# Performance work log

Hardware: AMD Instinct MI355X
Metric: run time of the kernel (lower is better)

## Reference

```python
import jax, jax.numpy as jnp
import numpy as np

N = 50000      # nodes
E = 600000     # edges
C = 128        # in_channels
H = 128        # hidden_channels
O = 128        # out_channels
G = 512        # graphs in batch
BN_EPS = 1e-5


def setup_inputs() -> dict:
    key = jax.random.key(0)
    ks = jax.random.split(key, 16)

    def w(k, shape):
        return jax.random.normal(k, shape, dtype=jnp.float32) * 0.05

    inp = {}
    inp["x"] = jax.random.normal(ks[0], (N, C), dtype=jnp.float32)
    inp["edge_index"] = jax.random.randint(ks[1], (2, E), 0, N, dtype=jnp.int64)
    inp["batch"] = jnp.sort(jax.random.randint(ks[2], (N,), 0, G, dtype=jnp.int64))

    dims = [(C, H, H), (H, H, H), (H, H, O)]
    ki = 3
    for li, (din, dh, dout) in enumerate(dims, 1):
        inp[f"g{li}_W1"] = w(ks[ki], (din, dh)); inp[f"g{li}_b1"] = jnp.zeros((dh,), jnp.float32)
        inp[f"g{li}_gm"] = jnp.ones((dh,), jnp.float32); inp[f"g{li}_bt"] = jnp.zeros((dh,), jnp.float32)
        inp[f"g{li}_rm"] = jnp.zeros((dh,), jnp.float32); inp[f"g{li}_rv"] = jnp.ones((dh,), jnp.float32)
        inp[f"g{li}_W2"] = w(ks[ki + 1], (dh, dout)); inp[f"g{li}_b2"] = jnp.zeros((dout,), jnp.float32)
        ki += 2
    inp["lin_W"] = w(ks[ki], (H + H + O, O))
    inp["lin_b"] = jnp.zeros((O,), jnp.float32)
    return inp


def gin_conv(x, src, dst, W1, b1, gm, bt, rm, rv, W2, b2):
    # GINConv (eps=0): mlp(x + sum_{j in N(i)} x_j); mlp = Linear-BN(eval)-ReLU-Linear
    agg = jax.ops.segment_sum(x[src], dst, num_segments=N)   # [N, d] scatter-add
    h = (x + agg) @ W1 + b1
    h = (h - rm) * jax.lax.rsqrt(rv + BN_EPS) * gm + bt      # BatchNorm1d, eval mode
    return jax.nn.relu(h) @ W2 + b2


def reference(x, edge_index, batch,
              g1_W1, g1_b1, g1_gm, g1_bt, g1_rm, g1_rv, g1_W2, g1_b2,
              g2_W1, g2_b1, g2_gm, g2_bt, g2_rm, g2_rv, g2_W2, g2_b2,
              g3_W1, g3_b1, g3_gm, g3_bt, g3_rm, g3_rv, g3_W2, g3_b2,
              lin_W, lin_b):
    src, dst = edge_index[0], edge_index[1]
    # dropout(0.2) is identity in eval mode
    x1 = jax.nn.relu(gin_conv(x, src, dst, g1_W1, g1_b1, g1_gm, g1_bt, g1_rm, g1_rv, g1_W2, g1_b2))
    x2 = jax.nn.relu(gin_conv(x1, src, dst, g2_W1, g2_b1, g2_gm, g2_bt, g2_rm, g2_rv, g2_W2, g2_b2))
    x3 = gin_conv(x2, src, dst, g3_W1, g3_b1, g3_gm, g3_bt, g3_rm, g3_rv, g3_W2, g3_b2)
    xc = jnp.concatenate([x1, x2, x3], axis=-1)              # JumpingKnowledge 'cat' -> [N, H+H+O]
    sums = jax.ops.segment_sum(xc, batch, num_segments=G)    # global_mean_pool
    cnt = jax.ops.segment_sum(jnp.ones((N, 1), xc.dtype), batch, num_segments=G)
    pooled = sums / jnp.maximum(cnt, 1.0)                    # [G, H+H+O]
    return pooled @ lin_W + lin_b                            # [G, O]
```

## Files before the change

### kernel.cpp

```cpp
#include <hip/hip_runtime.h>
#include <hip/hip_bf16.h>

#define NNODES 50000
#define NEDGES 600000
#define NGRAPHS 512
#define BN_EPS 1e-5f

typedef short bf16x8 __attribute__((ext_vector_type(8)));
typedef float f32x4 __attribute__((ext_vector_type(4)));

__device__ __forceinline__ void bf_split(float x, ushort& h, ushort& l) {
    __hip_bfloat16 bh = __float2bfloat16(x);
    float r = x - __bfloat162float(bh);
    __hip_bfloat16 bl = __float2bfloat16(r);
    h = __builtin_bit_cast(ushort, bh);
    l = __builtin_bit_cast(ushort, bl);
}
__device__ __forceinline__ ushort f2b(float x) {
    return __builtin_bit_cast(ushort, __float2bfloat16(x));
}
__device__ __forceinline__ float b2f(ushort u) {
    union { uint i; float f; } c; c.i = ((uint)u) << 16; return c.f;
}

__global__ __launch_bounds__(256) void prep_kernel(
    const float* __restrict__ x, ushort* __restrict__ xh,
    float* __restrict__ pooled, const int* __restrict__ dst,
    int* __restrict__ counts, int* __restrict__ row_ptr,
    const float* W0, const float* W1, const float* W2, const float* W3,
    const float* W4, const float* W5, ushort* __restrict__ hi, ushort* __restrict__ lo) {
    int b = blockIdx.x, t = threadIdx.x;
    if (b < 3125) {
        int f4 = b * 512 + t * 2;
        float4 a0 = ((const float4*)x)[f4];
        float4 a1 = ((const float4*)x)[f4 + 1];
        ushort4 u0 = {f2b(a0.x), f2b(a0.y), f2b(a0.z), f2b(a0.w)};
        ushort4 u1 = {f2b(a1.x), f2b(a1.y), f2b(a1.z), f2b(a1.w)};
        int e0 = f4 * 4;
        *(ushort4*)(xh + e0) = u0;
        *(ushort4*)(xh + e0 + 4) = u1;
        if (b == 0 && t == 0) row_ptr[NNODES] = NEDGES;
    } else if (b < 3317) {
        ((float4*)pooled)[(b - 3125) * 256 + t] = make_float4(0.f, 0.f, 0.f, 0.f);
    } else if (b < 5661) {
        int i = (b - 3317) * 256 + t;
        if (i < NEDGES) atomicAdd(&counts[dst[i]], 1);
    } else {
        int wb = b - 5661;
        const float* Ws[6] = {W0, W1, W2, W3, W4, W5};
        const float* W = Ws[wb >> 4];
        ushort* h = hi + (size_t)(wb >> 4) * 16384;
        ushort* l = lo + (size_t)(wb >> 4) * 16384;
        int chunk = wb & 15;
#pragma unroll
        for (int i = 0; i < 4; i++) {
            int idx = chunk * 1024 + i * 256 + t;
            int j    = idx & 7;
            int lane = (idx >> 3) & 63;
            int nt   = (idx >> 9) & 7;
            int kb   = (idx >> 12) & 3;
            int k = kb * 32 + ((lane >> 4) << 3) + j;
            int n = nt * 16 + (lane & 15);
            ushort hh, ll;
            bf_split(W[k * 128 + n], hh, ll);
            h[idx] = hh;
            l[idx] = ll;
        }
    }
}

__global__ __launch_bounds__(256) void scan1_kernel(const int* __restrict__ counts,
                                                    int* __restrict__ partials, int n) {
    __shared__ int s[256];
    int i = blockIdx.x * 256 + threadIdx.x;
    int v = (i < n) ? counts[i] : 0;
    s[threadIdx.x] = v;
    __syncthreads();
    for (int off = 128; off > 0; off >>= 1) {
        if (threadIdx.x < off) s[threadIdx.x] += s[threadIdx.x + off];
        __syncthreads();
    }
    if (threadIdx.x == 0) partials[blockIdx.x] = s[0];
}

__global__ __launch_bounds__(256) void scan3_kernel(const int* __restrict__ counts,
                                                    const int* __restrict__ partials,
                                                    int* __restrict__ row_ptr,
                                                    int* __restrict__ cursor, int n, int nb) {
    __shared__ int s[256];
    __shared__ int base_sh;
    int t = threadIdx.x;
    int pv = (t < (int)blockIdx.x && t < nb) ? partials[t] : 0;
    s[t] = pv;
    __syncthreads();
    for (int off = 128; off > 0; off >>= 1) {
        if (t < off) s[t] += s[t + off];
        __syncthreads();
    }
    if (t == 0) base_sh = s[0];
    __syncthreads();
    int base = base_sh;
    int i = blockIdx.x * 256 + t;
    int v = (i < n) ? counts[i] : 0;
    __syncthreads();
    s[t] = v;
    __syncthreads();
    for (int off = 1; off < 256; off <<= 1) {
        int nv = (t >= off) ? s[t - off] : 0;
        __syncthreads();
        s[t] += nv;
        __syncthreads();
    }
    if (i < n) {
        int ex = base + s[t] - v;
        row_ptr[i] = ex;
        cursor[i] = ex;
    }
}

__global__ __launch_bounds__(256) void scatter_kernel(const int* __restrict__ src,
                                                      const int* __restrict__ dst,
                                                      int* __restrict__ cursor,
                                                      int* __restrict__ esrc, int E) {
    int i = blockIdx.x * 256 + threadIdx.x;
    if (i < E) {
        int p = atomicAdd(&cursor[dst[i]], 1);
        esrc[p] = src[i];
    }
}

#define GB8(ACC, E0)                                                            \
    {                                                                           \
        int i0 = esrc[E0],     i1 = esrc[E0 + 1], i2 = esrc[E0 + 2], i3 = esrc[E0 + 3]; \
        int i4 = esrc[E0 + 4], i5 = esrc[E0 + 5], i6 = esrc[E0 + 6], i7 = esrc[E0 + 7]; \
        ushort4 v0 = xv[(size_t)i0 * 32 + q];                                   \
        ushort4 v1 = xv[(size_t)i1 * 32 + q];                                   \
        ushort4 v2 = xv[(size_t)i2 * 32 + q];                                   \
        ushort4 v3 = xv[(size_t)i3 * 32 + q];                                   \
        ushort4 v4 = xv[(size_t)i4 * 32 + q];                                   \
        ushort4 v5 = xv[(size_t)i5 * 32 + q];                                   \
        ushort4 v6 = xv[(size_t)i6 * 32 + q];                                   \
        ushort4 v7 = xv[(size_t)i7 * 32 + q];                                   \
        ACC.x += ((b2f(v0.x) + b2f(v1.x)) + (b2f(v2.x) + b2f(v3.x))) +          \
                 ((b2f(v4.x) + b2f(v5.x)) + (b2f(v6.x) + b2f(v7.x)));           \
        ACC.y += ((b2f(v0.y) + b2f(v1.y)) + (b2f(v2.y) + b2f(v3.y))) +          \
                 ((b2f(v4.y) + b2f(v5.y)) + (b2f(v6.y) + b2f(v7.y)));           \
        ACC.z += ((b2f(v0.z) + b2f(v1.z)) + (b2f(v2.z) + b2f(v3.z))) +          \
                 ((b2f(v4.z) + b2f(v5.z)) + (b2f(v6.z) + b2f(v7.z)));           \
        ACC.w += ((b2f(v0.w) + b2f(v1.w)) + (b2f(v2.w) + b2f(v3.w))) +          \
                 ((b2f(v4.w) + b2f(v5.w)) + (b2f(v6.w) + b2f(v7.w)));           \
    }

template <bool RELU_OUT, bool WRITE_PLANES>
__global__ __launch_bounds__(128) void layer_kernel(
    const ushort* __restrict__ Pin,
    const int* __restrict__ rp, const int* __restrict__ esrc,
    const ushort* __restrict__ W1hi, const ushort* __restrict__ W1lo,
    const ushort* __restrict__ W2hi, const ushort* __restrict__ W2lo,
    const float* __restrict__ b1, const float* __restrict__ gm,
    const float* __restrict__ bt, const float* __restrict__ rm,
    const float* __restrict__ rv, const float* __restrict__ b2,
    ushort* __restrict__ Ch,
    const int* __restrict__ batch, float* __restrict__ pooled, int poff, int M) {
    __shared__ __align__(16) ushort smem[64 * 136];
    __shared__ int bsm[64];
    const int t = threadIdx.x;
    const int lane = t & 63;
    const int wv = t >> 6;
    const int row0 = blockIdx.x * 64;
    const int g = lane >> 4, c = lane & 15;

    if (t < 64) bsm[t] = (row0 + t < M) ? batch[row0 + t] : -1;

    {
        const int hw = t >> 5;
        const int q  = t & 31;
        const ushort4* xv = (const ushort4*)Pin;
        for (int i = 0; i < 16; i += 2) {
            const int mA = hw * 16 + i, mB = mA + 1;
            const int nA = row0 + mA, nB = row0 + mB;
            float4 aA = make_float4(0.f, 0.f, 0.f, 0.f);
            float4 aB = make_float4(0.f, 0.f, 0.f, 0.f);
            int eA = 0, endA = 0, eB = 0, endB = 0;
            if (nA < M) {
                ushort4 s = xv[(size_t)nA * 32 + q];
                aA.x = b2f(s.x); aA.y = b2f(s.y); aA.z = b2f(s.z); aA.w = b2f(s.w);
                eA = rp[nA]; endA = rp[nA + 1];
            }
            if (nB < M) {
                ushort4 s = xv[(size_t)nB * 32 + q];
                aB.x = b2f(s.x); aB.y = b2f(s.y); aB.z = b2f(s.z); aB.w = b2f(s.w);
                eB = rp[nB]; endB = rp[nB + 1];
            }
            while (eA + 8 <= endA && eB + 8 <= endB) {
                int a0 = esrc[eA],     a1 = esrc[eA + 1], a2 = esrc[eA + 2], a3 = esrc[eA + 3];
                int a4 = esrc[eA + 4], a5 = esrc[eA + 5], a6 = esrc[eA + 6], a7 = esrc[eA + 7];
                int b0 = esrc[eB],     b1_ = esrc[eB + 1], b2_ = esrc[eB + 2], b3 = esrc[eB + 3];
                int b4 = esrc[eB + 4], b5 = esrc[eB + 5], b6 = esrc[eB + 6], b7 = esrc[eB + 7];
                ushort4 uA0 = xv[(size_t)a0 * 32 + q], uA1 = xv[(size_t)a1 * 32 + q];
                ushort4 uA2 = xv[(size_t)a2 * 32 + q], uA3 = xv[(size_t)a3 * 32 + q];
                ushort4 uA4 = xv[(size_t)a4 * 32 + q], uA5 = xv[(size_t)a5 * 32 + q];
                ushort4 uA6 = xv[(size_t)a6 * 32 + q], uA7 = xv[(size_t)a7 * 32 + q];
                ushort4 uB0 = xv[(size_t)b0 * 32 + q], uB1 = xv[(size_t)b1_ * 32 + q];
                ushort4 uB2 = xv[(size_t)b2_ * 32 + q], uB3 = xv[(size_t)b3 * 32 + q];
                ushort4 uB4 = xv[(size_t)b4 * 32 + q], uB5 = xv[(size_t)b5 * 32 + q];
                ushort4 uB6 = xv[(size_t)b6 * 32 + q], uB7 = xv[(size_t)b7 * 32 + q];
                aA.x += ((b2f(uA0.x) + b2f(uA1.x)) + (b2f(uA2.x) + b2f(uA3.x))) +
                        ((b2f(uA4.x) + b2f(uA5.x)) + (b2f(uA6.x) + b2f(uA7.x)));
                aA.y += ((b2f(uA0.y) + b2f(uA1.y)) + (b2f(uA2.y) + b2f(uA3.y))) +
                        ((b2f(uA4.y) + b2f(uA5.y)) + (b2f(uA6.y) + b2f(uA7.y)));
                aA.z += ((b2f(uA0.z) + b2f(uA1.z)) + (b2f(uA2.z) + b2f(uA3.z))) +
                        ((b2f(uA4.z) + b2f(uA5.z)) + (b2f(uA6.z) + b2f(uA7.z)));
                aA.w += ((b2f(uA0.w) + b2f(uA1.w)) + (b2f(uA2.w) + b2f(uA3.w))) +
                        ((b2f(uA4.w) + b2f(uA5.w)) + (b2f(uA6.w) + b2f(uA7.w)));
                aB.x += ((b2f(uB0.x) + b2f(uB1.x)) + (b2f(uB2.x) + b2f(uB3.x))) +
                        ((b2f(uB4.x) + b2f(uB5.x)) + (b2f(uB6.x) + b2f(uB7.x)));
                aB.y += ((b2f(uB0.y) + b2f(uB1.y)) + (b2f(uB2.y) + b2f(uB3.y))) +
                        ((b2f(uB4.y) + b2f(uB5.y)) + (b2f(uB6.y) + b2f(uB7.y)));
                aB.z += ((b2f(uB0.z) + b2f(uB1.z)) + (b2f(uB2.z) + b2f(uB3.z))) +
                        ((b2f(uB4.z) + b2f(uB5.z)) + (b2f(uB6.z) + b2f(uB7.z)));
                aB.w += ((b2f(uB0.w) + b2f(uB1.w)) + (b2f(uB2.w) + b2f(uB3.w))) +
                        ((b2f(uB4.w) + b2f(uB5.w)) + (b2f(uB6.w) + b2f(uB7.w)));
                eA += 8; eB += 8;
            }
            for (; eA + 8 <= endA; eA += 8) GB8(aA, eA);
            for (; eB + 8 <= endB; eB += 8) GB8(aB, eB);
            for (; eA + 2 <= endA; eA += 2) {
                int i0 = esrc[eA], i1 = esrc[eA + 1];
                ushort4 v0 = xv[(size_t)i0 * 32 + q];
                ushort4 v1 = xv[(size_t)i1 * 32 + q];
                aA.x += b2f(v0.x) + b2f(v1.x); aA.y += b2f(v0.y) + b2f(v1.y);
                aA.z += b2f(v0.z) + b2f(v1.z); aA.w += b2f(v0.w) + b2f(v1.w);
            }
            for (; eA < endA; eA++) {
                ushort4 v = xv[(size_t)esrc[eA] * 32 + q];
                aA.x += b2f(v.x); aA.y += b2f(v.y); aA.z += b2f(v.z); aA.w += b2f(v.w);
            }
            for (; eB + 2 <= endB; eB += 2) {
                int i0 = esrc[eB], i1 = esrc[eB + 1];
                ushort4 v0 = xv[(size_t)i0 * 32 + q];
                ushort4 v1 = xv[(size_t)i1 * 32 + q];
                aB.x += b2f(v0.x) + b2f(v1.x); aB.y += b2f(v0.y) + b2f(v1.y);
                aB.z += b2f(v0.z) + b2f(v1.z); aB.w += b2f(v0.w) + b2f(v1.w);
            }
            for (; eB < endB; eB++) {
                ushort4 v = xv[(size_t)esrc[eB] * 32 + q];
                aB.x += b2f(v.x); aB.y += b2f(v.y); aB.z += b2f(v.z); aB.w += b2f(v.w);
            }
            ushort4 hA = {f2b(aA.x), f2b(aA.y), f2b(aA.z), f2b(aA.w)};
            ushort4 hB = {f2b(aB.x), f2b(aB.y), f2b(aB.z), f2b(aB.w)};
            *(ushort4*)&smem[(q >> 3) * 2048 + mA * 32 + (q & 7) * 4] = hA;
            *(ushort4*)&smem[(q >> 3) * 2048 + mB * 32 + (q & 7) * 4] = hB;
        }
    }
    __syncthreads();

    f32x4 acc[4][4];
#pragma unroll
    for (int i = 0; i < 4; i++)
#pragma unroll
        for (int j = 0; j < 4; j++) acc[i][j] = (f32x4){0.f, 0.f, 0.f, 0.f};

    for (int kb = 0; kb < 4; kb++) {
        bf16x8 bh[4], bl[4];
#pragma unroll
        for (int ct = 0; ct < 4; ct++) {
            const size_t wo = (((size_t)kb * 8 + (wv * 4 + ct)) * 64 + lane) * 8;
            bh[ct] = *(const bf16x8*)(W1hi + wo);
            bl[ct] = *(const bf16x8*)(W1lo + wo);
        }
        bf16x8 ah[4];
#pragma unroll
        for (int rt = 0; rt < 4; rt++) {
            int off = kb * 2048 + (rt * 16 + c) * 32 + g * 8;
            ah[rt] = *(bf16x8*)&smem[off];
        }
#pragma unroll
        for (int rt = 0; rt < 4; rt++)
#pragma unroll
            for (int ct = 0; ct < 4; ct++) {
                acc[rt][ct] = __builtin_amdgcn_mfma_f32_16x16x32_bf16(ah[rt], bh[ct], acc[rt][ct], 0, 0, 0);
                acc[rt][ct] = __builtin_amdgcn_mfma_f32_16x16x32_bf16(ah[rt], bl[ct], acc[rt][ct], 0, 0, 0);
            }
    }
    __syncthreads();

    {
        float cs[4], ca[4];
#pragma unroll
        for (int ct = 0; ct < 4; ct++) {
            int n = wv * 64 + ct * 16 + c;
            float s = gm[n] * rsqrtf(rv[n] + BN_EPS);
            cs[ct] = s;
            ca[ct] = (b1[n] - rm[n]) * s + bt[n];
        }
#pragma unroll
        for (int rt = 0; rt < 4; rt++)
#pragma unroll
            for (int r = 0; r < 4; r++) {
                int row = rt * 16 + g * 4 + r;
#pragma unroll
                for (int ct = 0; ct < 4; ct++) {
                    int col = wv * 64 + ct * 16 + c;
                    float v = fmaxf(acc[rt][ct][r] * cs[ct] + ca[ct], 0.f);
                    smem[row * 136 + col] = f2b(v);
                }
            }
    }
    __syncthreads();

#pragma unroll
    for (int i = 0; i < 4; i++)
#pragma unroll
        for (int j = 0; j < 4; j++) acc[i][j] = (f32x4){0.f, 0.f, 0.f, 0.f};

    for (int kb = 0; kb < 4; kb++) {
        bf16x8 bh[4], bl[4];
#pragma unroll
        for (int ct = 0; ct < 4; ct++) {
            const size_t wo = (((size_t)kb * 8 + (wv * 4 + ct)) * 64 + lane) * 8;
            bh[ct] = *(const bf16x8*)(W2hi + wo);
            bl[ct] = *(const bf16x8*)(W2lo + wo);
        }
        bf16x8 ah[4];
#pragma unroll
        for (int rt = 0; rt < 4; rt++) {
            int off = (rt * 16 + c) * 136 + kb * 32 + g * 8;
            ah[rt] = *(bf16x8*)&smem[off];
        }
#pragma unroll
        for (int rt = 0; rt < 4; rt++)
#pragma unroll
            for (int ct = 0; ct < 4; ct++) {
                acc[rt][ct] = __builtin_amdgcn_mfma_f32_16x16x32_bf16(ah[rt], bh[ct], acc[rt][ct], 0, 0, 0);
                acc[rt][ct] = __builtin_amdgcn_mfma_f32_16x16x32_bf16(ah[rt], bl[ct], acc[rt][ct], 0, 0, 0);
            }
    }
    __syncthreads();

    {
        float ca2[4];
#pragma unroll
        for (int ct = 0; ct < 4; ct++) ca2[ct] = b2[wv * 64 + ct * 16 + c];
#pragma unroll
        for (int rt = 0; rt < 4; rt++)
#pragma unroll
            for (int r = 0; r < 4; r++) {
                int rl = rt * 16 + g * 4 + r;
                int row = row0 + rl;
                bool valid = row < M;
#pragma unroll
                for (int ct = 0; ct < 4; ct++) {
                    int col = wv * 64 + ct * 16 + c;
                    float v = acc[rt][ct][r] + ca2[ct];
                    if (RELU_OUT) v = fmaxf(v, 0.f);
                    ushort hh = f2b(valid ? v : 0.f);
                    smem[rl * 136 + col] = hh;
                    if (WRITE_PLANES && valid) Ch[(size_t)row * 128 + col] = hh;
                }
            }
    }
    __syncthreads();

    {
        int col = t;
        int gcur = bsm[0];
        float accp = 0.f;
#pragma unroll 8
        for (int r = 0; r < 64; r++) {
            int gg = bsm[r];
            if (gg != gcur) {
                if (gcur >= 0) atomicAdd(&pooled[gcur * 384 + poff + col], accp);
                accp = 0.f;
                gcur = gg;
            }
            accp += b2f(smem[r * 136 + col]);
        }
        if (gcur >= 0) atomicAdd(&pooled[gcur * 384 + poff + col], accp);
    }
}

__global__ __launch_bounds__(128) void final_kernel(const float* __restrict__ pooled,
                                                    const int* __restrict__ batch,
                                                    const float* __restrict__ W,
                                                    const float* __restrict__ b,
                                                    float* __restrict__ out, int n) {
    __shared__ float ps[384];
    int gph = blockIdx.x, t = threadIdx.x;
    int lo1 = 0, hi1 = n;
    while (lo1 < hi1) { int mid = (lo1 + hi1) >> 1; if (batch[mid] < gph) lo1 = mid + 1; else hi1 = mid; }
    int start = lo1;
    int lo2 = start, hi2 = n;
    while (lo2 < hi2) { int mid = (lo2 + hi2) >> 1; if (batch[mid] < gph + 1) lo2 = mid + 1; else hi2 = mid; }
    int cnt = lo2 - start;
    float inv = 1.f / (float)(cnt > 0 ? cnt : 1);
    for (int i = t; i < 384; i += 128) ps[i] = pooled[gph * 384 + i] * inv;
    __syncthreads();
    float acc = b[t];
#pragma unroll 8
    for (int k = 0; k < 384; k++) acc += ps[k] * W[k * 128 + t];
    out[gph * 128 + t] = acc;
}

extern "C" void kernel_launch(void* const* d_in, const int* in_sizes, int n_in,
                              void* d_out, int out_size, void* d_ws, size_t ws_size,
                              hipStream_t stream) {
    const float* x     = (const float*)d_in[0];
    const int*   edge  = (const int*)d_in[1];
    const int*   batch = (const int*)d_in[2];
    const float* p[32];
    for (int i = 0; i < n_in && i < 32; i++) p[i] = (const float*)d_in[i];
    const float* lin_W = p[27];
    const float* lin_b = p[28];

    char* w = (char*)d_ws;
    auto alloc = [&](size_t bytes) { void* r = (void*)w; w += (bytes + 255) & ~(size_t)255; return r; };
    const size_t PL = (size_t)NNODES * 128;
    ushort* xh0   = (ushort*)alloc(PL * 2);
    ushort* p1h   = (ushort*)alloc(PL * 2);
    ushort* p2h   = xh0;
    float* pooled = (float*)alloc((size_t)NGRAPHS * 384 * 4);
    int* counts   = (int*)alloc((size_t)NNODES * 4);
    int* cursor   = (int*)alloc((size_t)NNODES * 4);
    int* row_ptr  = (int*)alloc((size_t)(NNODES + 1) * 4);
    int* esrc     = (int*)alloc((size_t)NEDGES * 4);
    int* partials = (int*)alloc(256 * 4);
    ushort* wt_hi = (ushort*)alloc((size_t)6 * 16384 * 2);
    ushort* wt_lo = (ushort*)alloc((size_t)6 * 16384 * 2);

    const int* src = edge;
    const int* dst = edge + NEDGES;

    hipMemsetAsync(counts, 0, (size_t)NNODES * 4, stream);
    prep_kernel<<<5757, 256, 0, stream>>>(x, xh0, pooled, dst, counts, row_ptr,
                                          p[3], p[9], p[11], p[17], p[19], p[25],
                                          wt_hi, wt_lo);

    int nb = (NNODES + 255) / 256;
    scan1_kernel<<<nb, 256, 0, stream>>>(counts, partials, NNODES);
    scan3_kernel<<<nb, 256, 0, stream>>>(counts, partials, row_ptr, cursor, NNODES, nb);
    scatter_kernel<<<(NEDGES + 255) / 256, 256, 0, stream>>>(src, dst, cursor, esrc, NEDGES);

    int grid = (NNODES + 63) / 64;
    layer_kernel<true, true><<<grid, 128, 0, stream>>>(xh0, row_ptr, esrc,
        wt_hi + 0 * 16384, wt_lo + 0 * 16384, wt_hi + 1 * 16384, wt_lo + 1 * 16384,
        p[4], p[5], p[6], p[7], p[8], p[10], p1h, batch, pooled, 0, NNODES);
    layer_kernel<true, true><<<grid, 128, 0, stream>>>(p1h, row_ptr, esrc,
        wt_hi + 2 * 16384, wt_lo + 2 * 16384, wt_hi + 3 * 16384, wt_lo + 3 * 16384,
        p[12], p[13], p[14], p[15], p[16], p[18], p2h, batch, pooled, 128, NNODES);
    layer_kernel<false, false><<<grid, 128, 0, stream>>>(p2h, row_ptr, esrc,
        wt_hi + 4 * 16384, wt_lo + 4 * 16384, wt_hi + 5 * 16384, wt_lo + 5 * 16384,
        p[20], p[21], p[22], p[23], p[24], p[26], nullptr, batch, pooled, 256, NNODES);

    final_kernel<<<NGRAPHS, 128, 0, stream>>>(pooled, batch, lin_W, lin_b,
                                              (float*)d_out, NNODES);
}
```

Baseline: 411.5 us.

## Widen gather loads to 16 bytes, use 4 waves per block, fuse scan

The neighbor gather now reads 8 bf16 values per lane with uint4 loads, so 16 lanes cover a row instead of 32. This makes fewer, wider memory transactions. Each layer block now runs 4 waves (256 threads) instead of 2, and each wave computes a 32-column MFMA slice instead of 64. That lowers per-thread accumulator registers and puts more waves in flight. The two-pass scan is merged into one kernel that recomputes the prefix of the counts on every block, removing a launch but doing redundant reads that grow with the block index.

```diff
diff --git a/kernel.cpp b/kernel.cpp
--- a/kernel.cpp
+++ b/kernel.cpp
@@ -22,6 +22,64 @@
 __device__ __forceinline__ float b2f(ushort u) {
     union { uint i; float f; } c; c.i = ((uint)u) << 16; return c.f;
 }
+__device__ __forceinline__ float blo(uint u) {
+    union { uint i; float f; } c; c.i = u << 16; return c.f;
+}
+__device__ __forceinline__ float bhi(uint u) {
+    union { uint i; float f; } c; c.i = u & 0xffff0000u; return c.f;
+}
+
+#define TREE8(A, v0, v1, v2, v3, v4, v5, v6, v7)                               \
+    A[0] += ((blo(v0.x) + blo(v1.x)) + (blo(v2.x) + blo(v3.x))) +              \
+            ((blo(v4.x) + blo(v5.x)) + (blo(v6.x) + blo(v7.x)));               \
+    A[1] += ((bhi(v0.x) + bhi(v1.x)) + (bhi(v2.x) + bhi(v3.x))) +              \
+            ((bhi(v4.x) + bhi(v5.x)) + (bhi(v6.x) + bhi(v7.x)));               \
+    A[2] += ((blo(v0.y) + blo(v1.y)) + (blo(v2.y) + blo(v3.y))) +              \
+            ((blo(v4.y) + blo(v5.y)) + (blo(v6.y) + blo(v7.y)));               \
+    A[3] += ((bhi(v0.y) + bhi(v1.y)) + (bhi(v2.y) + bhi(v3.y))) +              \
+            ((bhi(v4.y) + bhi(v5.y)) + (bhi(v6.y) + bhi(v7.y)));               \
+    A[4] += ((blo(v0.z) + blo(v1.z)) + (blo(v2.z) + blo(v3.z))) +              \
+            ((blo(v4.z) + blo(v5.z)) + (blo(v6.z) + blo(v7.z)));               \
+    A[5] += ((bhi(v0.z) + bhi(v1.z)) + (bhi(v2.z) + bhi(v3.z))) +              \
+            ((bhi(v4.z) + bhi(v5.z)) + (bhi(v6.z) + bhi(v7.z)));               \
+    A[6] += ((blo(v0.w) + blo(v1.w)) + (blo(v2.w) + blo(v3.w))) +              \
+            ((blo(v4.w) + blo(v5.w)) + (blo(v6.w) + blo(v7.w)));               \
+    A[7] += ((bhi(v0.w) + bhi(v1.w)) + (bhi(v2.w) + bhi(v3.w))) +              \
+            ((bhi(v4.w) + bhi(v5.w)) + (bhi(v6.w) + bhi(v7.w)));
+
+#define GB8U(A, E)                                                             \
+    {                                                                          \
+        int i0 = esrc[E],     i1 = esrc[E + 1], i2 = esrc[E + 2], i3 = esrc[E + 3]; \
+        int i4 = esrc[E + 4], i5 = esrc[E + 5], i6 = esrc[E + 6], i7 = esrc[E + 7]; \
+        uint4 v0 = xv[(size_t)i0 * 16 + q];                                    \
+        uint4 v1 = xv[(size_t)i1 * 16 + q];                                    \
+        uint4 v2 = xv[(size_t)i2 * 16 + q];                                    \
+        uint4 v3 = xv[(size_t)i3 * 16 + q];                                    \
+        uint4 v4 = xv[(size_t)i4 * 16 + q];                                    \
+        uint4 v5 = xv[(size_t)i5 * 16 + q];                                    \
+        uint4 v6 = xv[(size_t)i6 * 16 + q];                                    \
+        uint4 v7 = xv[(size_t)i7 * 16 + q];                                    \
+        TREE8(A, v0, v1, v2, v3, v4, v5, v6, v7)                               \
+    }
+
+#define GB2U(A, E)                                                             \
+    {                                                                          \
+        int i0 = esrc[E], i1 = esrc[E + 1];                                    \
+        uint4 v0 = xv[(size_t)i0 * 16 + q];                                    \
+        uint4 v1 = xv[(size_t)i1 * 16 + q];                                    \
+        A[0] += blo(v0.x) + blo(v1.x); A[1] += bhi(v0.x) + bhi(v1.x);          \
+        A[2] += blo(v0.y) + blo(v1.y); A[3] += bhi(v0.y) + bhi(v1.y);          \
+        A[4] += blo(v0.z) + blo(v1.z); A[5] += bhi(v0.z) + bhi(v1.z);          \
+        A[6] += blo(v0.w) + blo(v1.w); A[7] += bhi(v0.w) + bhi(v1.w);          \
+    }
+#define GB1U(A, E)                                                             \
+    {                                                                          \
+        uint4 v = xv[(size_t)esrc[E] * 16 + q];                                \
+        A[0] += blo(v.x); A[1] += bhi(v.x);                                    \
+        A[2] += blo(v.y); A[3] += bhi(v.y);                                    \
+        A[4] += blo(v.z); A[5] += bhi(v.z);                                    \
+        A[6] += blo(v.w); A[7] += bhi(v.w);                                    \
+    }
 
 __global__ __launch_bounds__(256) void prep_kernel(
     const float* __restrict__ x, ushort* __restrict__ xh,
@@ -69,29 +127,16 @@
     }
 }
 
-__global__ __launch_bounds__(256) void scan1_kernel(const int* __restrict__ counts,
-                                                    int* __restrict__ partials, int n) {
-    __shared__ int s[256];
-    int i = blockIdx.x * 256 + threadIdx.x;
-    int v = (i < n) ? counts[i] : 0;
-    s[threadIdx.x] = v;
-    __syncthreads();
-    for (int off = 128; off > 0; off >>= 1) {
-        if (threadIdx.x < off) s[threadIdx.x] += s[threadIdx.x + off];
-        __syncthreads();
-    }
-    if (threadIdx.x == 0) partials[blockIdx.x] = s[0];
-}
-
-__global__ __launch_bounds__(256) void scan3_kernel(const int* __restrict__ counts,
-                                                    const int* __restrict__ partials,
-                                                    int* __restrict__ row_ptr,
-                                                    int* __restrict__ cursor, int n, int nb) {
+__global__ __launch_bounds__(256) void scan_kernel(const int* __restrict__ counts,
+                                                   int* __restrict__ row_ptr,
+                                                   int* __restrict__ cursor, int n) {
     __shared__ int s[256];
     __shared__ int base_sh;
     int t = threadIdx.x;
-    int pv = (t < (int)blockIdx.x && t < nb) ? partials[t] : 0;
-    s[t] = pv;
+    int start = blockIdx.x * 256;
+    int partial = 0;
+    for (int i = t; i < start; i += 256) partial += counts[i];
+    s[t] = partial;
     __syncthreads();
     for (int off = 128; off > 0; off >>= 1) {
         if (t < off) s[t] += s[t + off];
@@ -100,7 +145,7 @@
     if (t == 0) base_sh = s[0];
     __syncthreads();
     int base = base_sh;
-    int i = blockIdx.x * 256 + t;
+    int i = start + t;
     int v = (i < n) ? counts[i] : 0;
     __syncthreads();
     s[t] = v;
@@ -129,30 +174,8 @@
     }
 }
 
-#define GB8(ACC, E0)                                                            \
-    {                                                                           \
-        int i0 = esrc[E0],     i1 = esrc[E0 + 1], i2 = esrc[E0 + 2], i3 = esrc[E0 + 3]; \
-        int i4 = esrc[E0 + 4], i5 = esrc[E0 + 5], i6 = esrc[E0 + 6], i7 = esrc[E0 + 7]; \
-        ushort4 v0 = xv[(size_t)i0 * 32 + q];                                   \
-        ushort4 v1 = xv[(size_t)i1 * 32 + q];                                   \
-        ushort4 v2 = xv[(size_t)i2 * 32 + q];                                   \
-        ushort4 v3 = xv[(size_t)i3 * 32 + q];                                   \
-        ushort4 v4 = xv[(size_t)i4 * 32 + q];                                   \
-        ushort4 v5 = xv[(size_t)i5 * 32 + q];                                   \
-        ushort4 v6 = xv[(size_t)i6 * 32 + q];                                   \
-        ushort4 v7 = xv[(size_t)i7 * 32 + q];                                   \
-        ACC.x += ((b2f(v0.x) + b2f(v1.x)) + (b2f(v2.x) + b2f(v3.x))) +          \
-                 ((b2f(v4.x) + b2f(v5.x)) + (b2f(v6.x) + b2f(v7.x)));           \
-        ACC.y += ((b2f(v0.y) + b2f(v1.y)) + (b2f(v2.y) + b2f(v3.y))) +          \
-                 ((b2f(v4.y) + b2f(v5.y)) + (b2f(v6.y) + b2f(v7.y)));           \
-        ACC.z += ((b2f(v0.z) + b2f(v1.z)) + (b2f(v2.z) + b2f(v3.z))) +          \
-                 ((b2f(v4.z) + b2f(v5.z)) + (b2f(v6.z) + b2f(v7.z)));           \
-        ACC.w += ((b2f(v0.w) + b2f(v1.w)) + (b2f(v2.w) + b2f(v3.w))) +          \
-                 ((b2f(v4.w) + b2f(v5.w)) + (b2f(v6.w) + b2f(v7.w)));           \
-    }
-
 template <bool RELU_OUT, bool WRITE_PLANES>
-__global__ __launch_bounds__(128) void layer_kernel(
+__global__ __launch_bounds__(256) void layer_kernel(
     const ushort* __restrict__ Pin,
     const int* __restrict__ rp, const int* __restrict__ esrc,
     const ushort* __restrict__ W1hi, const ushort* __restrict__ W1lo,
@@ -173,23 +196,29 @@
     if (t < 64) bsm[t] = (row0 + t < M) ? batch[row0 + t] : -1;
 
     {
-        const int hw = t >> 5;
-        const int q  = t & 31;
-        const ushort4* xv = (const ushort4*)Pin;
-        for (int i = 0; i < 16; i += 2) {
-            const int mA = hw * 16 + i, mB = mA + 1;
+        const int grp = lane >> 4;
+        const int q   = lane & 15;
+        const uint4* xv = (const uint4*)Pin;
+        for (int it = 0; it < 2; it++) {
+            const int mA = wv * 16 + it * 8 + grp * 2, mB = mA + 1;
             const int nA = row0 + mA, nB = row0 + mB;
-            float4 aA = make_float4(0.f, 0.f, 0.f, 0.f);
-            float4 aB = make_float4(0.f, 0.f, 0.f, 0.f);
+            float aA[8] = {0.f, 0.f, 0.f, 0.f, 0.f, 0.f, 0.f, 0.f};
+            float aB[8] = {0.f, 0.f, 0.f, 0.f, 0.f, 0.f, 0.f, 0.f};
             int eA = 0, endA = 0, eB = 0, endB = 0;
             if (nA < M) {
-                ushort4 s = xv[(size_t)nA * 32 + q];
-                aA.x = b2f(s.x); aA.y = b2f(s.y); aA.z = b2f(s.z); aA.w = b2f(s.w);
+                uint4 s0 = xv[(size_t)nA * 16 + q];
+                aA[0] = blo(s0.x); aA[1] = bhi(s0.x);
+                aA[2] = blo(s0.y); aA[3] = bhi(s0.y);
+                aA[4] = blo(s0.z); aA[5] = bhi(s0.z);
+                aA[6] = blo(s0.w); aA[7] = bhi(s0.w);
                 eA = rp[nA]; endA = rp[nA + 1];
             }
             if (nB < M) {
-                ushort4 s = xv[(size_t)nB * 32 + q];
-                aB.x = b2f(s.x); aB.y = b2f(s.y); aB.z = b2f(s.z); aB.w = b2f(s.w);
+                uint4 s0 = xv[(size_t)nB * 16 + q];
+                aB[0] = blo(s0.x); aB[1] = bhi(s0.x);
+                aB[2] = blo(s0.y); aB[3] = bhi(s0.y);
+                aB[4] = blo(s0.z); aB[5] = bhi(s0.z);
+                aB[6] = blo(s0.w); aB[7] = bhi(s0.w);
                 eB = rp[nB]; endB = rp[nB + 1];
             }
             while (eA + 8 <= endA && eB + 8 <= endB) {
@@ -197,75 +226,50 @@
                 int a4 = esrc[eA + 4], a5 = esrc[eA + 5], a6 = esrc[eA + 6], a7 = esrc[eA + 7];
                 int b0 = esrc[eB],     b1_ = esrc[eB + 1], b2_ = esrc[eB + 2], b3 = esrc[eB + 3];
                 int b4 = esrc[eB + 4], b5 = esrc[eB + 5], b6 = esrc[eB + 6], b7 = esrc[eB + 7];
-                ushort4 uA0 = xv[(size_t)a0 * 32 + q], uA1 = xv[(size_t)a1 * 32 + q];
-                ushort4 uA2 = xv[(size_t)a2 * 32 + q], uA3 = xv[(size_t)a3 * 32 + q];
-                ushort4 uA4 = xv[(size_t)a4 * 32 + q], uA5 = xv[(size_t)a5 * 32 + q];
-                ushort4 uA6 = xv[(size_t)a6 * 32 + q], uA7 = xv[(size_t)a7 * 32 + q];
-                ushort4 uB0 = xv[(size_t)b0 * 32 + q], uB1 = xv[(size_t)b1_ * 32 + q];
-                ushort4 uB2 = xv[(size_t)b2_ * 32 + q], uB3 = xv[(size_t)b3 * 32 + q];
-                ushort4 uB4 = xv[(size_t)b4 * 32 + q], uB5 = xv[(size_t)b5 * 32 + q];
-                ushort4 uB6 = xv[(size_t)b6 * 32 + q], uB7 = xv[(size_t)b7 * 32 + q];
-                aA.x += ((b2f(uA0.x) + b2f(uA1.x)) + (b2f(uA2.x) + b2f(uA3.x))) +
-                        ((b2f(uA4.x) + b2f(uA5.x)) + (b2f(uA6.x) + b2f(uA7.x)));
-                aA.y += ((b2f(uA0.y) + b2f(uA1.y)) + (b2f(uA2.y) + b2f(uA3.y))) +
-                        ((b2f(uA4.y) + b2f(uA5.y)) + (b2f(uA6.y) + b2f(uA7.y)));
-                aA.z += ((b2f(uA0.z) + b2f(uA1.z)) + (b2f(uA2.z) + b2f(uA3.z))) +
-                        ((b2f(uA4.z) + b2f(uA5.z)) + (b2f(uA6.z) + b2f(uA7.z)));
-                aA.w += ((b2f(uA0.w) + b2f(uA1.w)) + (b2f(uA2.w) + b2f(uA3.w))) +
-                        ((b2f(uA4.w) + b2f(uA5.w)) + (b2f(uA6.w) + b2f(uA7.w)));
-                aB.x += ((b2f(uB0.x) + b2f(uB1.x)) + (b2f(uB2.x) + b2f(uB3.x))) +
-                        ((b2f(uB4.x) + b2f(uB5.x)) + (b2f(uB6.x) + b2f(uB7.x)));
-                aB.y += ((b2f(uB0.y) + b2f(uB1.y)) + (b2f(uB2.y) + b2f(uB3.y))) +
-                        ((b2f(uB4.y) + b2f(uB5.y)) + (b2f(uB6.y) + b2f(uB7.y)));
-                aB.z += ((b2f(uB0.z) + b2f(uB1.z)) + (b2f(uB2.z) + b2f(uB3.z))) +
-                        ((b2f(uB4.z) + b2f(uB5.z)) + (b2f(uB6.z) + b2f(uB7.z)));
-                aB.w += ((b2f(uB0.w) + b2f(uB1.w)) + (b2f(uB2.w) + b2f(uB3.w))) +
-                        ((b2f(uB4.w) + b2f(uB5.w)) + (b2f(uB6.w) + b2f(uB7.w)));
+                uint4 vA0 = xv[(size_t)a0 * 16 + q], vA1 = xv[(size_t)a1 * 16 + q];
+                uint4 vA2 = xv[(size_t)a2 * 16 + q], vA3 = xv[(size_t)a3 * 16 + q];
+                uint4 vA4 = xv[(size_t)a4 * 16 + q], vA5 = xv[(size_t)a5 * 16 + q];
+                uint4 vA6 = xv[(size_t)a6 * 16 + q], vA7 = xv[(size_t)a7 * 16 + q];
+                uint4 vB0 = xv[(size_t)b0 * 16 + q], vB1 = xv[(size_t)b1_ * 16 + q];
+                uint4 vB2 = xv[(size_t)b2_ * 16 + q], vB3 = xv[(size_t)b3 * 16 + q];
+                uint4 vB4 = xv[(size_t)b4 * 16 + q], vB5 = xv[(size_t)b5 * 16 + q];
+                uint4 vB6 = xv[(size_t)b6 * 16 + q], vB7 = xv[(size_t)b7 * 16 + q];
+                TREE8(aA, vA0, vA1, vA2, vA3, vA4, vA5, vA6, vA7)
+                TREE8(aB, vB0, vB1, vB2, vB3, vB4, vB5, vB6, vB7)
                 eA += 8; eB += 8;
             }
-            for (; eA + 8 <= endA; eA += 8) GB8(aA, eA);
-            for (; eB + 8 <= endB; eB += 8) GB8(aB, eB);
-            for (; eA + 2 <= endA; eA += 2) {
-                int i0 = esrc[eA], i1 = esrc[eA + 1];
-                ushort4 v0 = xv[(size_t)i0 * 32 + q];
-                ushort4 v1 = xv[(size_t)i1 * 32 + q];
-                aA.x += b2f(v0.x) + b2f(v1.x); aA.y += b2f(v0.y) + b2f(v1.y);
-                aA.z += b2f(v0.z) + b2f(v1.z); aA.w += b2f(v0.w) + b2f(v1.w);
-            }
-            for (; eA < endA; eA++) {
-                ushort4 v = xv[(size_t)esrc[eA] * 32 + q];
-                aA.x += b2f(v.x); aA.y += b2f(v.y); aA.z += b2f(v.z); aA.w += b2f(v.w);
-            }
-            for (; eB + 2 <= endB; eB += 2) {
-                int i0 = esrc[eB], i1 = esrc[eB + 1];
-                ushort4 v0 = xv[(size_t)i0 * 32 + q];
-                ushort4 v1 = xv[(size_t)i1 * 32 + q];
-                aB.x += b2f(v0.x) + b2f(v1.x); aB.y += b2f(v0.y) + b2f(v1.y);
-                aB.z += b2f(v0.z) + b2f(v1.z); aB.w += b2f(v0.w) + b2f(v1.w);
-            }
-            for (; eB < endB; eB++) {
-                ushort4 v = xv[(size_t)esrc[eB] * 32 + q];
-                aB.x += b2f(v.x); aB.y += b2f(v.y); aB.z += b2f(v.z); aB.w += b2f(v.w);
-            }
-            ushort4 hA = {f2b(aA.x), f2b(aA.y), f2b(aA.z), f2b(aA.w)};
-            ushort4 hB = {f2b(aB.x), f2b(aB.y), f2b(aB.z), f2b(aB.w)};
-            *(ushort4*)&smem[(q >> 3) * 2048 + mA * 32 + (q & 7) * 4] = hA;
-            *(ushort4*)&smem[(q >> 3) * 2048 + mB * 32 + (q & 7) * 4] = hB;
-        }
-    }
-    __syncthreads();
-
-    f32x4 acc[4][4];
+            for (; eA + 8 <= endA; eA += 8) GB8U(aA, eA);
+            for (; eB + 8 <= endB; eB += 8) GB8U(aB, eB);
+            for (; eA + 2 <= endA; eA += 2) GB2U(aA, eA);
+            for (; eA < endA; eA++) GB1U(aA, eA);
+            for (; eB + 2 <= endB; eB += 2) GB2U(aB, eB);
+            for (; eB < endB; eB++) GB1U(aB, eB);
+            uint4 oA, oB;
+            oA.x = (uint)f2b(aA[0]) | ((uint)f2b(aA[1]) << 16);
+            oA.y = (uint)f2b(aA[2]) | ((uint)f2b(aA[3]) << 16);
+            oA.z = (uint)f2b(aA[4]) | ((uint)f2b(aA[5]) << 16);
+            oA.w = (uint)f2b(aA[6]) | ((uint)f2b(aA[7]) << 16);
+            oB.x = (uint)f2b(aB[0]) | ((uint)f2b(aB[1]) << 16);
+            oB.y = (uint)f2b(aB[2]) | ((uint)f2b(aB[3]) << 16);
+            oB.z = (uint)f2b(aB[4]) | ((uint)f2b(aB[5]) << 16);
+            oB.w = (uint)f2b(aB[6]) | ((uint)f2b(aB[7]) << 16);
+            *(uint4*)&smem[(q >> 2) * 2048 + mA * 32 + (q & 3) * 8] = oA;
+            *(uint4*)&smem[(q >> 2) * 2048 + mB * 32 + (q & 3) * 8] = oB;
+        }
+    }
+    __syncthreads();
+
+    f32x4 acc[4][2];
 #pragma unroll
     for (int i = 0; i < 4; i++)
 #pragma unroll
-        for (int j = 0; j < 4; j++) acc[i][j] = (f32x4){0.f, 0.f, 0.f, 0.f};
+        for (int j = 0; j < 2; j++) acc[i][j] = (f32x4){0.f, 0.f, 0.f, 0.f};
 
     for (int kb = 0; kb < 4; kb++) {
-        bf16x8 bh[4], bl[4];
-#pragma unroll
-        for (int ct = 0; ct < 4; ct++) {
-            const size_t wo = (((size_t)kb * 8 + (wv * 4 + ct)) * 64 + lane) * 8;
+        bf16x8 bh[2], bl[2];
+#pragma unroll
+        for (int ct = 0; ct < 2; ct++) {
+            const size_t wo = (((size_t)kb * 8 + (wv * 2 + ct)) * 64 + lane) * 8;
             bh[ct] = *(const bf16x8*)(W1hi + wo);
             bl[ct] = *(const bf16x8*)(W1lo + wo);
         }
@@ -278,7 +282,7 @@
 #pragma unroll
         for (int rt = 0; rt < 4; rt++)
 #pragma unroll
-            for (int ct = 0; ct < 4; ct++) {
+            for (int ct = 0; ct < 2; ct++) {
                 acc[rt][ct] = __builtin_amdgcn_mfma_f32_16x16x32_bf16(ah[rt], bh[ct], acc[rt][ct], 0, 0, 0);
                 acc[rt][ct] = __builtin_amdgcn_mfma_f32_16x16x32_bf16(ah[rt], bl[ct], acc[rt][ct], 0, 0, 0);
             }
@@ -286,10 +290,10 @@
     __syncthreads();
 
     {
-        float cs[4], ca[4];
-#pragma unroll
-        for (int ct = 0; ct < 4; ct++) {
-            int n = wv * 64 + ct * 16 + c;
+        float cs[2], ca[2];
+#pragma unroll
+        for (int ct = 0; ct < 2; ct++) {
+            int n = wv * 32 + ct * 16 + c;
             float s = gm[n] * rsqrtf(rv[n] + BN_EPS);
             cs[ct] = s;
             ca[ct] = (b1[n] - rm[n]) * s + bt[n];
@@ -300,8 +304,8 @@
             for (int r = 0; r < 4; r++) {
                 int row = rt * 16 + g * 4 + r;
 #pragma unroll
-                for (int ct = 0; ct < 4; ct++) {
-                    int col = wv * 64 + ct * 16 + c;
+                for (int ct = 0; ct < 2; ct++) {
+                    int col = wv * 32 + ct * 16 + c;
                     float v = fmaxf(acc[rt][ct][r] * cs[ct] + ca[ct], 0.f);
                     smem[row * 136 + col] = f2b(v);
                 }
@@ -312,13 +316,13 @@
 #pragma unroll
     for (int i = 0; i < 4; i++)
 #pragma unroll
-        for (int j = 0; j < 4; j++) acc[i][j] = (f32x4){0.f, 0.f, 0.f, 0.f};
+        for (int j = 0; j < 2; j++) acc[i][j] = (f32x4){0.f, 0.f, 0.f, 0.f};
 
     for (int kb = 0; kb < 4; kb++) {
-        bf16x8 bh[4], bl[4];
-#pragma unroll
-        for (int ct = 0; ct < 4; ct++) {
-            const size_t wo = (((size_t)kb * 8 + (wv * 4 + ct)) * 64 + lane) * 8;
+        bf16x8 bh[2], bl[2];
+#pragma unroll
+        for (int ct = 0; ct < 2; ct++) {
+            const size_t wo = (((size_t)kb * 8 + (wv * 2 + ct)) * 64 + lane) * 8;
             bh[ct] = *(const bf16x8*)(W2hi + wo);
             bl[ct] = *(const bf16x8*)(W2lo + wo);
         }
@@ -331,7 +335,7 @@
 #pragma unroll
         for (int rt = 0; rt < 4; rt++)
 #pragma unroll
-            for (int ct = 0; ct < 4; ct++) {
+            for (int ct = 0; ct < 2; ct++) {
                 acc[rt][ct] = __builtin_amdgcn_mfma_f32_16x16x32_bf16(ah[rt], bh[ct], acc[rt][ct], 0, 0, 0);
                 acc[rt][ct] = __builtin_amdgcn_mfma_f32_16x16x32_bf16(ah[rt], bl[ct], acc[rt][ct], 0, 0, 0);
             }
@@ -339,9 +343,9 @@
     __syncthreads();
 
     {
-        float ca2[4];
-#pragma unroll
-        for (int ct = 0; ct < 4; ct++) ca2[ct] = b2[wv * 64 + ct * 16 + c];
+        float ca2[2];
+#pragma unroll
+        for (int ct = 0; ct < 2; ct++) ca2[ct] = b2[wv * 32 + ct * 16 + c];
 #pragma unroll
         for (int rt = 0; rt < 4; rt++)
 #pragma unroll
@@ -350,8 +354,8 @@
                 int row = row0 + rl;
                 bool valid = row < M;
 #pragma unroll
-                for (int ct = 0; ct < 4; ct++) {
-                    int col = wv * 64 + ct * 16 + c;
+                for (int ct = 0; ct < 2; ct++) {
+                    int col = wv * 32 + ct * 16 + c;
                     float v = acc[rt][ct][r] + ca2[ct];
                     if (RELU_OUT) v = fmaxf(v, 0.f);
                     ushort hh = f2b(valid ? v : 0.f);
@@ -362,7 +366,7 @@
     }
     __syncthreads();
 
-    {
+    if (t < 128) {
         int col = t;
         int gcur = bsm[0];
         float accp = 0.f;
@@ -424,7 +428,6 @@
     int* cursor   = (int*)alloc((size_t)NNODES * 4);
     int* row_ptr  = (int*)alloc((size_t)(NNODES + 1) * 4);
     int* esrc     = (int*)alloc((size_t)NEDGES * 4);
-    int* partials = (int*)alloc(256 * 4);
     ushort* wt_hi = (ushort*)alloc((size_t)6 * 16384 * 2);
     ushort* wt_lo = (ushort*)alloc((size_t)6 * 16384 * 2);
 
@@ -437,18 +440,17 @@
                                           wt_hi, wt_lo);
 
     int nb = (NNODES + 255) / 256;
-    scan1_kernel<<<nb, 256, 0, stream>>>(counts, partials, NNODES);
-    scan3_kernel<<<nb, 256, 0, stream>>>(counts, partials, row_ptr, cursor, NNODES, nb);
+    scan_kernel<<<nb, 256, 0, stream>>>(counts, row_ptr, cursor, NNODES);
     scatter_kernel<<<(NEDGES + 255) / 256, 256, 0, stream>>>(src, dst, cursor, esrc, NEDGES);
 
     int grid = (NNODES + 63) / 64;
-    layer_kernel<true, true><<<grid, 128, 0, stream>>>(xh0, row_ptr, esrc,
+    layer_kernel<true, true><<<grid, 256, 0, stream>>>(xh0, row_ptr, esrc,
         wt_hi + 0 * 16384, wt_lo + 0 * 16384, wt_hi + 1 * 16384, wt_lo + 1 * 16384,
         p[4], p[5], p[6], p[7], p[8], p[10], p1h, batch, pooled, 0, NNODES);
-    layer_kernel<true, true><<<grid, 128, 0, stream>>>(p1h, row_ptr, esrc,
+    layer_kernel<true, true><<<grid, 256, 0, stream>>>(p1h, row_ptr, esrc,
         wt_hi + 2 * 16384, wt_lo + 2 * 16384, wt_hi + 3 * 16384, wt_lo + 3 * 16384,
         p[12], p[13], p[14], p[15], p[16], p[18], p2h, batch, pooled, 128, NNODES);
-    layer_kernel<false, false><<<grid, 128, 0, stream>>>(p2h, row_ptr, esrc,
+    layer_kernel<false, false><<<grid, 256, 0, stream>>>(p2h, row_ptr, esrc,
         wt_hi + 4 * 16384, wt_lo + 4 * 16384, wt_hi + 5 * 16384, wt_lo + 5 * 16384,
         p[20], p[21], p[22], p[23], p[24], p[26], nullptr, batch, pooled, 256, NNODES);
 
```

After: 405.4 us. No clear change (-1.5%).
